# Performance work log

Hardware: AMD Instinct MI355X
Metric: run time of the kernel (lower is better)

## Reference

```python
import jax, jax.numpy as jnp
import numpy as np

# ---- fixed constants from stft2hcfp.__init__ ----
FS = 16000.0; FR = 2.0; FC = 27.5; TC = 1.0 / 4487.0; NPO = 48
N = int(FS / FR)                      # 8000 FFT length
HALF_N = int(round(N / 2))            # 4000
SQRT_N = float(np.sqrt(N))
HIGH_FREQ_IDX = int(round(1.0 / TC / FR) + 1)   # 2245
HIGH_QUEF_IDX = int(round(FS / FC)) + 1         # 583
CUT_Q = int(round(FS * TC))           # 4  (cepstrum cutoff)
TOTAL_BINS = 4 * 88                   # 352 log-freq bins
NUM_HARMONIC = 5

def _central_freqs():
    stop = 1.0 / TC
    nest = int(np.ceil(np.log2(stop / FC)) * NPO)
    cf = []
    for i in range(nest):
        c = FC * 2.0 ** (float(i) / NPO)
        if c < stop:
            cf.append(c)
        else:
            break
    return cf

CF = _central_freqs()   # 353 central frequencies
NEST = len(CF)

def _freq_matrix():
    # triangular log-frequency filterbank over linear freq axis
    f = (FS * np.linspace(0, 0.5, HALF_N, endpoint=True))[:HIGH_FREQ_IDX]
    W = np.zeros((NEST - 1, len(f)), np.float32)
    for i in range(1, NEST - 1):
        l = int(round(CF[i - 1] / FR)); r = int(round(CF[i + 1] / FR) + 1)
        if l >= r - 1:
            W[i, l] = 1.0
        else:
            for j in range(l, r):
                if CF[i - 1] < f[j] < CF[i]:
                    W[i, j] = (f[j] - CF[i - 1]) / (CF[i] - CF[i - 1])
                elif CF[i] < f[j] < CF[i + 1]:
                    W[i, j] = (CF[i + 1] - f[j]) / (CF[i + 1] - CF[i])
    return W

def _quef_matrix():
    q = np.arange(HIGH_QUEF_IDX) / FS + 1e-6
    fq = 1.0 / q
    W = np.zeros((NEST - 1, len(fq)), np.float32)
    for i in range(1, NEST - 1):
        for j in range(int(round(FS / CF[i + 1])), int(round(FS / CF[i - 1]) + 1)):
            if j >= len(fq):
                continue
            if CF[i - 1] < fq[j] < CF[i]:
                W[i, j] = (fq[j] - CF[i - 1]) / (CF[i] - CF[i - 1])
            elif CF[i] < fq[j] < CF[i + 1]:
                W[i, j] = (CF[i + 1] - fq[j]) / (CF[i + 1] - CF[i])
    return W

# harmonic shift indices: closest central freq to (k+1)*27.5 Hz, k=0..5
HIDS = [int(np.argmin(np.abs(np.asarray(CF) - (k + 1) * FC))) for k in range(NUM_HARMONIC + 1)]


def _nonlinear(x, g, cutoff):
    # relu + pow(g), then zero first/last `cutoff` rows along axis 1.
    # safe pow: grad is 0 where x<=0 (matches relu-masked torch behavior, no inf at 0)
    y = jnp.where(x > 0, jnp.where(x > 0, x, 1.0) ** g, 0.0)
    y = y.at[:, :cutoff].set(0.0).at[:, -cutoff:].set(0.0)
    return y


def setup_inputs() -> dict:
    key = jax.random.key(0)
    dx = jax.random.uniform(key, (8, 512, N), dtype=jnp.float32)  # [B, T, 8000] spectrogram
    return {
        "dx": dx,
        "W_freq": jnp.asarray(_freq_matrix()),   # [352, 2245]
        "W_quef": jnp.asarray(_quef_matrix()),   # [352, 583]
    }


def reference(dx, W_freq, W_quef):
    tfr0 = jnp.swapaxes(dx, 1, 2)                       # [B, F=8000, T]
    # CFP layer 1: real part of FFT over freq axis -> cepstrum, nonlinear g=0.6
    ceps = jnp.fft.fft(tfr0, axis=1).real / SQRT_N      # [B, 8000, T]
    ceps = _nonlinear(ceps, 0.6, CUT_Q)
    # log-frequency mappings (banded triangular filterbanks)
    tfr0h = tfr0[:, :HIGH_FREQ_IDX]                      # [B, 2245, T]
    cepsh = ceps[:, :HIGH_QUEF_IDX]                      # [B, 583, T]
    tfrL0 = jnp.einsum('kf,bft->bkt', W_freq, tfr0h)     # [B, 352, T]
    tfrLQ = jnp.einsum('kq,bqt->bkt', W_quef, cepsh)     # [B, 352, T]
    # harmonic stacking: shift down (spectral) / shift up (cepstral)
    har_s = [jnp.pad(tfrL0[:, h:TOTAL_BINS], ((0, 0), (0, h), (0, 0))) for h in HIDS]
    har_c = [jnp.pad(tfrLQ[:, :TOTAL_BINS - h], ((0, 0), (h, 0), (0, 0))) for h in HIDS]
    piece = jnp.concatenate([jnp.stack(har_s, axis=1), jnp.stack(har_c, axis=1)], axis=1)
    return jnp.swapaxes(piece, 2, 3)                     # [B, 12, T, 352]
```

## Files before the change

kernel.cpp:

```cpp
#include <hip/hip_runtime.h>
#include <hip/hip_bf16.h>
#include <limits.h>

typedef __attribute__((ext_vector_type(8))) short short8;
typedef __attribute__((ext_vector_type(4))) float f32x4;
typedef __attribute__((ext_vector_type(16))) float f32x16;

#define NN 8000
#define NCOL 4096
#define KBINS 352
#define QPAD 640
#define QH 160
#define BN 128
#define KC 4
#define NTILE 64
#define KSTEP 16
#define CUTQ 4
#define T_ 512
#define WFB 64
#define WQB 20

#define GLL16(g, l) __builtin_amdgcn_global_load_lds( \
    (const __attribute__((address_space(1))) unsigned int*)(g), \
    (__attribute__((address_space(3))) unsigned int*)(l), 16, 0, 0)

static __device__ __forceinline__ ushort bfc(float f){
  __hip_bfloat16 h = __float2bfloat16(f);
  return *reinterpret_cast<ushort*>(&h);
}
static __device__ __forceinline__ float b2f(ushort u){
  unsigned v = ((unsigned)u) << 16; float f; __builtin_memcpy(&f, &v, 4); return f;
}

__global__ void gen_cos_k(ushort* __restrict__ cosg, int HQI){
  int n = blockIdx.x*256 + threadIdx.x;
  int q = blockIdx.y;
  float v = 0.f;
  if (q < HQI){
    int m = (q*n) % NN;
    v = cosf((float)m * 7.8539816339744831e-4f);
  }
  int kt = n >> 6, s8 = (n >> 3) & 7, e = n & 7;
  cosg[(size_t)kt*(QPAD*64) + (size_t)q*64 + (((s8 ^ (q & 7)) << 3) | e)] = bfc(v);
}

#define PADI(j) ((j) + ((j) >> 5))
__global__ __launch_bounds__(512) void fold_k(const float* __restrict__ dx,
                                              ushort* __restrict__ xf){
  __shared__ float sbuf[4232];
  int row = blockIdx.x;
  int t = threadIdx.x;
  const float* rp = dx + (size_t)row*NN;

  {
    int j0 = t*8;
    f32x4 v0 = *(const f32x4*)(rp + 3896 + j0);
    f32x4 v1 = *(const f32x4*)(rp + 3896 + j0 + 4);
    #pragma unroll
    for (int e=0;e<4;e++) sbuf[PADI(j0+e)] = v0[e];
    #pragma unroll
    for (int e=0;e<4;e++) sbuf[PADI(j0+4+e)] = v1[e];
    if (t == 0){
      #pragma unroll
      for (int e=0;e<8;e++) sbuf[PADI(4096+e)] = rp[7992+e];
    }
  }
  __syncthreads();

  int n0 = t*8;
  f32x4 p0 = *(const f32x4*)(rp + n0);
  f32x4 p1 = *(const f32x4*)(rp + n0 + 4);
  float pr[8] = {p0[0],p0[1],p0[2],p0[3],p1[0],p1[1],p1[2],p1[3]};
  short8 o;
  #pragma unroll
  for (int e=0;e<8;e++){
    int n = n0 + e;
    float v;
    if (n == 0)          v = pr[0];
    else if (n < 4000)   v = pr[e] + sbuf[PADI(4104 - n)];
    else if (n == 4000)  v = pr[e];
    else                 v = 0.f;
    o[e] = (short)bfc(v);
  }
  int kt = n0 >> 6, s8 = (n0 >> 3) & 7;
  *(short8*)(&xf[((size_t)kt*NCOL + row)*64 + ((s8 ^ (row & 7)) << 3)]) = o;
}

__global__ void bounds_k(const float* __restrict__ W, int width,
                         int* __restrict__ lo, int* __restrict__ hi){
  __shared__ int slo, shi;
  int r = blockIdx.x;
  if (threadIdx.x==0){ slo = INT_MAX; shi = -1; }
  __syncthreads();
  int mylo = INT_MAX, myhi = -1;
  for (int c = threadIdx.x; c < width; c += 256){
    if (W[(size_t)r*width + c] != 0.f){ if (c < mylo) mylo = c; if (c > myhi) myhi = c; }
  }
  atomicMin(&slo, mylo); atomicMax(&shi, myhi);
  __syncthreads();
  if (threadIdx.x==0){
    if (shi < 0){ lo[r] = 0; hi[r] = 0; }
    else        { lo[r] = slo; hi[r] = shi + 1; }
  }
}

__global__ void pack_k(const float* __restrict__ W, const int* __restrict__ lo,
                       const int* __restrict__ hi, int width, int bw,
                       float* __restrict__ WT){
  int r = blockIdx.x;
  int l = lo[r], h = hi[r];
  for (int j = threadIdx.x; j < bw; j += 64){
    float v = 0.f;
    if (l + j < h) v = W[(size_t)r*width + l + j];
    WT[(size_t)j*KBINS + r] = v;
  }
}

__global__ __launch_bounds__(256, 2) void gemm_k(const ushort* __restrict__ xf,
                                                 const ushort* __restrict__ cosg,
                                                 ushort* __restrict__ part){
  __shared__ ushort As[2][QH*64];
  __shared__ ushort Bs[2][BN*64];
  int tid = threadIdx.x;
  int nb = blockIdx.x, qh = blockIdx.y, kc = blockIdx.z;
  int lane = tid & 63, wn = tid >> 6;
  int l31 = lane & 31, lh = lane >> 5;
  int kt0 = kc*KSTEP, ktE = kt0 + KSTEP;

  const ushort* ag0 = cosg + (size_t)qh*(QH*64) + tid*8;
  const ushort* bg0 = xf + (size_t)nb*(BN*64) + tid*8;

  #define STAGE(kt_, buf_) { \
    const ushort* ag_ = ag0 + (size_t)(kt_)*(QPAD*64); \
    _Pragma("unroll") \
    for (int i_=0;i_<5;i_++) GLL16(ag_ + i_*2048, &As[buf_][tid*8 + i_*2048]); \
    const ushort* bg_ = bg0 + (size_t)(kt_)*(NCOL*64); \
    _Pragma("unroll") \
    for (int i_=0;i_<4;i_++) GLL16(bg_ + i_*2048, &Bs[buf_][tid*8 + i_*2048]); }

  f32x16 acc[5];
  #pragma unroll
  for (int a=0;a<5;a++) acc[a] = (f32x16)0.f;

  STAGE(kt0, 0);
  __syncthreads();

  int cur = 0;
  for (int kt = kt0; kt < ktE; ++kt){
    if (kt + 1 < ktE) STAGE(kt+1, cur^1);
    const ushort* Ac = &As[cur][0];
    const ushort* Bc = &Bs[cur][0];
    #pragma unroll
    for (int p=0;p<4;p++){
      int brow = wn*32 + l31;
      short8 dfr = *(const short8*)(Bc + brow*64 + ((((p<<1)|lh) ^ (brow & 7)) << 3));
      short8 cfr[5];
      #pragma unroll
      for (int a=0;a<5;a++){
        int arow = a*32 + l31;
        cfr[a] = *(const short8*)(Ac + arow*64 + ((((p<<1)|lh) ^ (arow & 7)) << 3));
      }
      __builtin_amdgcn_s_setprio(1);
      #pragma unroll
      for (int a=0;a<5;a++)
        acc[a] = __builtin_amdgcn_mfma_f32_32x32x16_bf16(dfr, cfr[a], acc[a], 0,0,0);
      __builtin_amdgcn_s_setprio(0);
    }
    __syncthreads();
    cur ^= 1;
  }

  ushort* pb = part + (size_t)kc*NCOL*QPAD;
  #pragma unroll
  for (int a=0;a<5;a++){
    int q = qh*QH + a*32 + l31;
    int colb = nb*BN + wn*32 + 4*lh;
    #pragma unroll
    for (int r=0;r<16;r++){
      int col = colb + (r&3) + 8*(r>>2);
      pb[(size_t)col*QPAD + q] = bfc(acc[a][r]);
    }
  }
}

__global__ __launch_bounds__(384) void fuse_k(const float* __restrict__ dx,
        const ushort* __restrict__ part,
        const float* __restrict__ WfT, const float* __restrict__ WqT,
        const int* __restrict__ fLo, const int* __restrict__ qLo,
        float* __restrict__ out, int HFI, int HQI){
  __shared__ float xr[2368];
  __shared__ float yq[QPAD];
  __shared__ float tl0[KBINS];
  __shared__ float tlq[KBINS];
  int col = blockIdx.x;
  int b = col >> 9, t = col & 511;
  int tid = threadIdx.x;
  const float invs = 0.011180339887498949f;

  for (int f = tid; f < 2368; f += 384) xr[f] = (f < HFI) ? dx[(size_t)col*NN + f] : 0.f;
  const ushort* pc = part + (size_t)col*QPAD;
  for (int q = tid; q < QPAD; q += 384){
    float y = 0.f;
    if (q < HQI){
      float s = 0.f;
      #pragma unroll
      for (int kc=0; kc<KC; kc++) s += b2f(pc[(size_t)kc*NCOL*QPAD + q]);
      s *= invs;
      if (q >= CUTQ && s > 0.f) y = powf(s, 0.6f);
    }
    yq[q] = y;
  }
  __syncthreads();

  if (tid < KBINS){
    int k = tid;
    int lo = fLo[k];
    float aF = 0.f;
    #pragma unroll
    for (int j=0;j<WFB;j++) aF += WfT[j*KBINS + k] * xr[lo + j];
    int ql = qLo[k];
    float aQ = 0.f;
    #pragma unroll
    for (int j=0;j<WQB;j++) aQ += WqT[j*KBINS + k] * yq[ql + j];
    tl0[k] = aF; tlq[k] = aQ;
  }
  __syncthreads();

  const int hids[6] = {0,48,76,96,111,124};
  for (int u = tid; u < 12*KBINS; u += 384){
    int j = u / KBINS;
    int k = u - j*KBINS;
    int h = hids[(j < 6) ? j : j - 6];
    float v;
    if (j < 6) v = (k + h < KBINS) ? tl0[k + h] : 0.f;
    else       v = (k >= h)        ? tlq[k - h] : 0.f;
    out[(((size_t)b*12 + j)*T_ + t)*KBINS + k] = v;
  }
}

extern "C" void kernel_launch(void* const* d_in, const int* in_sizes, int n_in,
                              void* d_out, int out_size, void* d_ws, size_t ws_size,
                              hipStream_t stream){
  const float* dx = (const float*)d_in[0];
  const float* Wf = (const float*)d_in[1];
  const float* Wq = (const float*)d_in[2];
  int HFI = in_sizes[1] / KBINS;
  int HQI = in_sizes[2] / KBINS;
  float* out = (float*)d_out;
  char* ws = (char*)d_ws;

  ushort* cosg = (ushort*)ws;
  size_t off = (size_t)NTILE*QPAD*64*2;
  ushort* xf = (ushort*)(ws + off); off += (size_t)NTILE*NCOL*64*2;
  ushort* part = (ushort*)(ws + off); off += (size_t)KC*NCOL*QPAD*2;
  int* fLo = (int*)(ws+off); off += KBINS*4;
  int* fHi = (int*)(ws+off); off += KBINS*4;
  int* qLo = (int*)(ws+off); off += KBINS*4;
  int* qHi = (int*)(ws+off); off += KBINS*4;
  float* WfT = (float*)(ws+off); off += (size_t)WFB*KBINS*4;
  float* WqT = (float*)(ws+off); off += (size_t)WQB*KBINS*4;
  (void)n_in; (void)out_size; (void)ws_size;

  gen_cos_k<<<dim3(16, QPAD), 256, 0, stream>>>(cosg, HQI);
  fold_k<<<NCOL, 512, 0, stream>>>(dx, xf);
  bounds_k<<<KBINS, 256, 0, stream>>>(Wf, HFI, fLo, fHi);
  bounds_k<<<KBINS, 256, 0, stream>>>(Wq, HQI, qLo, qHi);
  pack_k<<<KBINS, 64, 0, stream>>>(Wf, fLo, fHi, HFI, WFB, WfT);
  pack_k<<<KBINS, 64, 0, stream>>>(Wq, qLo, qHi, HQI, WQB, WqT);
  gemm_k<<<dim3(NCOL/BN, QPAD/QH, KC), 256, 0, stream>>>(xf, cosg, part);
  fuse_k<<<NCOL, 384, 0, stream>>>(dx, part, WfT, WqT, fLo, qLo, out, HFI, HQI);
}
```

Measured before the change: 138.2 us.

## Merge filterbank prep kernels and overlap GEMM prefetch with explicit vmcnt waits

The four bounds/pack launches become one kernel over a 2D grid that finds each row's nonzero band and writes the transposed band, dropping three launches and the hi arrays. In the GEMM main loop the full __syncthreads after staging is replaced by a partial s_waitcnt vmcnt(9), so only the previous tile's global-to-LDS loads are awaited while the next tile's nine loads stay in flight. Raw s_barrier plus sched_barrier pin instruction order. This depends on the hand-counted outstanding-load number matching the compiler's issued loads, otherwise LDS reads could race.

```diff
diff --git a/kernel.cpp b/kernel.cpp
--- a/kernel.cpp
+++ b/kernel.cpp
@@ -51,7 +51,6 @@
   int row = blockIdx.x;
   int t = threadIdx.x;
   const float* rp = dx + (size_t)row*NN;
-
   {
     int j0 = t*8;
     f32x4 v0 = *(const f32x4*)(rp + 3896 + j0);
@@ -86,10 +85,17 @@
   *(short8*)(&xf[((size_t)kt*NCOL + row)*64 + ((s8 ^ (row & 7)) << 3)]) = o;
 }
 
-__global__ void bounds_k(const float* __restrict__ W, int width,
-                         int* __restrict__ lo, int* __restrict__ hi){
+__global__ void bp_k(const float* __restrict__ Wf, const float* __restrict__ Wq,
+                     int HFI, int HQI, int* __restrict__ fLo, int* __restrict__ qLo,
+                     float* __restrict__ WfT, float* __restrict__ WqT){
   __shared__ int slo, shi;
   int r = blockIdx.x;
+  bool isF = (blockIdx.y == 0);
+  const float* W = isF ? Wf : Wq;
+  int width = isF ? HFI : HQI;
+  int bw    = isF ? WFB : WQB;
+  float* WT = isF ? WfT : WqT;
+  int* Lo   = isF ? fLo : qLo;
   if (threadIdx.x==0){ slo = INT_MAX; shi = -1; }
   __syncthreads();
   int mylo = INT_MAX, myhi = -1;
@@ -98,18 +104,9 @@
   }
   atomicMin(&slo, mylo); atomicMax(&shi, myhi);
   __syncthreads();
-  if (threadIdx.x==0){
-    if (shi < 0){ lo[r] = 0; hi[r] = 0; }
-    else        { lo[r] = slo; hi[r] = shi + 1; }
-  }
-}
-
-__global__ void pack_k(const float* __restrict__ W, const int* __restrict__ lo,
-                       const int* __restrict__ hi, int width, int bw,
-                       float* __restrict__ WT){
-  int r = blockIdx.x;
-  int l = lo[r], h = hi[r];
-  for (int j = threadIdx.x; j < bw; j += 64){
+  int l = (shi < 0) ? 0 : slo, h = (shi < 0) ? 0 : shi + 1;
+  if (threadIdx.x==0) Lo[r] = l;
+  for (int j = threadIdx.x; j < bw; j += 256){
     float v = 0.f;
     if (l + j < h) v = W[(size_t)r*width + l + j];
     WT[(size_t)j*KBINS + r] = v;
@@ -143,11 +140,18 @@
   for (int a=0;a<5;a++) acc[a] = (f32x16)0.f;
 
   STAGE(kt0, 0);
-  __syncthreads();
 
   int cur = 0;
   for (int kt = kt0; kt < ktE; ++kt){
-    if (kt + 1 < ktE) STAGE(kt+1, cur^1);
+    bool stg = (kt + 1 < ktE);
+    if (stg){
+      STAGE(kt+1, cur^1);
+      asm volatile("s_waitcnt vmcnt(9)" ::: "memory");
+    } else {
+      asm volatile("s_waitcnt vmcnt(0)" ::: "memory");
+    }
+    __builtin_amdgcn_s_barrier();
+    __builtin_amdgcn_sched_barrier(0);
     const ushort* Ac = &As[cur][0];
     const ushort* Bc = &Bs[cur][0];
     #pragma unroll
@@ -166,7 +170,9 @@
         acc[a] = __builtin_amdgcn_mfma_f32_32x32x16_bf16(dfr, cfr[a], acc[a], 0,0,0);
       __builtin_amdgcn_s_setprio(0);
     }
-    __syncthreads();
+    __builtin_amdgcn_sched_barrier(0);
+    __builtin_amdgcn_s_barrier();
+    __builtin_amdgcn_sched_barrier(0);
     cur ^= 1;
   }
 
@@ -254,19 +260,14 @@
   ushort* xf = (ushort*)(ws + off); off += (size_t)NTILE*NCOL*64*2;
   ushort* part = (ushort*)(ws + off); off += (size_t)KC*NCOL*QPAD*2;
   int* fLo = (int*)(ws+off); off += KBINS*4;
-  int* fHi = (int*)(ws+off); off += KBINS*4;
   int* qLo = (int*)(ws+off); off += KBINS*4;
-  int* qHi = (int*)(ws+off); off += KBINS*4;
   float* WfT = (float*)(ws+off); off += (size_t)WFB*KBINS*4;
   float* WqT = (float*)(ws+off); off += (size_t)WQB*KBINS*4;
   (void)n_in; (void)out_size; (void)ws_size;
 
   gen_cos_k<<<dim3(16, QPAD), 256, 0, stream>>>(cosg, HQI);
   fold_k<<<NCOL, 512, 0, stream>>>(dx, xf);
-  bounds_k<<<KBINS, 256, 0, stream>>>(Wf, HFI, fLo, fHi);
-  bounds_k<<<KBINS, 256, 0, stream>>>(Wq, HQI, qLo, qHi);
-  pack_k<<<KBINS, 64, 0, stream>>>(Wf, fLo, fHi, HFI, WFB, WfT);
-  pack_k<<<KBINS, 64, 0, stream>>>(Wq, qLo, qHi, HQI, WQB, WqT);
+  bp_k<<<dim3(KBINS, 2), 256, 0, stream>>>(Wf, Wq, HFI, HQI, fLo, qLo, WfT, WqT);
   gemm_k<<<dim3(NCOL/BN, QPAD/QH, KC), 256, 0, stream>>>(xf, cosg, part);
   fuse_k<<<NCOL, 384, 0, stream>>>(dx, part, WfT, WqT, fLo, qLo, out, HFI, HQI);
 }
```

After: 129.4 us. -6.4%, faster.
